# Kernel tuning notes

Measured on AMD Instinct MI355X. Metric: run time of the kernel, lower is better.

## Reference

```python
import jax, jax.numpy as jnp
import numpy as np

# Parallel-beam CT geometry constants (unit pitch, centered detector/volume)
VOXEL_W = 1.0   # voxel width (mm) == integration step along the ray
PIXEL_W = 1.0   # detector column pitch (mm)
N_T = 384       # ray samples, ~ sqrt(2) * 256 to cover the volume diagonal


def setup_inputs() -> dict:
    key = jax.random.key(0)
    vol = jax.random.normal(key, (1, 32, 256, 256), dtype=jnp.float32)  # [B, Z, Y, X]
    phis = jnp.arange(180, dtype=jnp.float32)  # view angles in degrees
    return {"vol": vol, "phis": phis}


def _project(vol, phis_deg):
    """Ray-driven parallel-beam forward projection with bilinear interpolation.

    vol: [B, Z, Y, X] attenuation volume.
    Returns sinogram g: [B, nAngles, nRows=Z, nCols=X].
    """
    B, Z, Y, X = vol.shape
    nCols = X
    dtype = vol.dtype
    centerCol = (nCols - 1) / 2.0
    # detector-column lateral offsets and ray-parameter samples (world coords)
    u = (jnp.arange(nCols, dtype=dtype) - centerCol) * PIXEL_W          # [nCols]
    t = (jnp.arange(N_T, dtype=dtype) - (N_T - 1) / 2.0) * VOXEL_W      # [nT]
    phis = phis_deg * (jnp.pi / 180.0)
    cs = jnp.stack([jnp.cos(phis), jnp.sin(phis)], axis=-1)             # [nAngles, 2]

    def bilinear(ix, iy):
        # ix, iy: fractional voxel coords, shape [nT, nCols]
        ix0f = jnp.floor(ix); iy0f = jnp.floor(iy)
        fx = ix - ix0f; fy = iy - iy0f
        ix0 = ix0f.astype(jnp.int32); iy0 = iy0f.astype(jnp.int32)
        ix1 = ix0 + 1; iy1 = iy0 + 1

        def valid_clip(i, n):
            v = (i >= 0) & (i <= n - 1)
            return v, jnp.clip(i, 0, n - 1)

        vx0, jx0 = valid_clip(ix0, X); vx1, jx1 = valid_clip(ix1, X)
        vy0, jy0 = valid_clip(iy0, Y); vy1, jy1 = valid_clip(iy1, Y)
        zero = jnp.zeros((), dtype)
        wx0 = jnp.where(vx0, 1.0 - fx, zero); wx1 = jnp.where(vx1, fx, zero)
        wy0 = jnp.where(vy0, 1.0 - fy, zero); wy1 = jnp.where(vy1, fy, zero)
        # gathers broadcast over [B, Z]; result [B, Z, nT, nCols]
        return (wy0 * (wx0 * vol[..., jy0, jx0] + wx1 * vol[..., jy0, jx1])
              + wy1 * (wx0 * vol[..., jy1, jx0] + wx1 * vol[..., jy1, jx1]))

    def one_angle(carry, cs_a):
        c, s = cs_a[0], cs_a[1]
        # world (x, y) sample positions along each detector column's ray
        x = u[None, :] * (-s) + t[:, None] * c   # [nT, nCols]
        y = u[None, :] * c + t[:, None] * s
        ix = x / VOXEL_W + (X - 1) / 2.0
        iy = y / VOXEL_W + (Y - 1) / 2.0
        vals = bilinear(ix, iy)                  # [B, Z, nT, nCols]
        g = vals.sum(axis=2) * VOXEL_W           # line integral -> [B, Z, nCols]
        return carry, g

    _, g = jax.lax.scan(one_angle, 0, cs)        # [nAngles, B, Z, nCols]
    return jnp.transpose(g, (1, 0, 2, 3))        # [B, nAngles, Z, nCols]


def reference(vol, phis):
    return _project(vol, phis)
```

## Files before the change

kernel.cpp:

```cpp
#include <hip/hip_runtime.h>
#include <hip/hip_fp16.h>

#define XDIM 256
#define YDIM 256
#define ZDIM 32
#define NT 384
#define NA 180
#define AG 2
#define SW 263
#define SR 70
#define CELLS (SR * SW)
#define SMEM_BYTES 147280

__global__ __launch_bounds__(1024) void proj_kernel(
    const float* __restrict__ vol, const float* __restrict__ phis,
    float* __restrict__ out) {
  extern __shared__ char smem[];
  uint2* sl = reinterpret_cast<uint2*>(smem);
  float4* ps = reinterpret_cast<float4*>(smem);

  const int tid = threadIdx.x;
  const int zq = blockIdx.x;
  const int ag = blockIdx.y;
  const int col = tid & 255;
  const int q = tid >> 8;
  const float u = (float)col - 127.5f;

  const float phi0 = phis[ag * AG] * 0.017453292519943295f;
  const int ax = (fabsf(sinf(phi0)) >= fabsf(cosf(phi0))) ? 1 : 0;

  float c_[AG], s_[AG];
#pragma unroll
  for (int j = 0; j < AG; ++j) {
    const float phi = phis[ag * AG + j] * 0.017453292519943295f;
    c_[j] = cosf(phi);
    s_[j] = sinf(phi);
  }
  float4 acc[AG];
#pragma unroll
  for (int j = 0; j < AG; ++j) acc[j] = make_float4(0.f, 0.f, 0.f, 0.f);

  const float* vb = vol + (zq * 4) * (YDIM * XDIM);

#pragma unroll
  for (int st = 0; st < 4; ++st) {
    const int gr0 = st * 64 - 3;
    __syncthreads();

    if (tid < SR * 7) {
      int r = tid / 7;
      int c7 = tid - r * 7;
      int lw = c7 < 3 ? c7 : c7 + 256;
      sl[r * SW + lw] = make_uint2(0u, 0u);
    }
    if (ax) {
      for (int i = 0; i < 18; ++i) {
        int k = tid + (i << 10);
        if (k < SR * 256) {
          int r = k >> 8, x = k & 255, gr = gr0 + r;
          uint2 v = make_uint2(0u, 0u);
          if ((unsigned)gr < 256u) {
            int gi = gr * XDIM + x;
            __half2 p = __floats2half2_rn(vb[gi], vb[gi + 65536]);
            __half2 qq = __floats2half2_rn(vb[gi + 131072], vb[gi + 196608]);
            v.x = *reinterpret_cast<unsigned*>(&p);
            v.y = *reinterpret_cast<unsigned*>(&qq);
          }
          sl[r * SW + x + 3] = v;
        }
      }
    } else {
      for (int i = 0; i < 16; ++i) {
        int k = tid + (i << 10);
        int r = k & 63, y = k >> 6, gx = gr0 + r;
        uint2 v = make_uint2(0u, 0u);
        if ((unsigned)gx < 256u) {
          int gi = y * XDIM + gx;
          __half2 p = __floats2half2_rn(vb[gi], vb[gi + 65536]);
          __half2 qq = __floats2half2_rn(vb[gi + 131072], vb[gi + 196608]);
          v.x = *reinterpret_cast<unsigned*>(&p);
          v.y = *reinterpret_cast<unsigned*>(&qq);
        }
        sl[r * SW + y + 3] = v;
      }
      for (int i = 0; i < 2; ++i) {
        int k = tid + (i << 10);
        int rb = k & 7, y = k >> 3;
        if (rb < 6) {
          int r = 64 + rb, gx = gr0 + r;
          uint2 v = make_uint2(0u, 0u);
          if ((unsigned)gx < 256u) {
            int gi = y * XDIM + gx;
            __half2 p = __floats2half2_rn(vb[gi], vb[gi + 65536]);
            __half2 qq = __floats2half2_rn(vb[gi + 131072], vb[gi + 196608]);
            v.x = *reinterpret_cast<unsigned*>(&p);
            v.y = *reinterpret_cast<unsigned*>(&qq);
          }
          sl[r * SW + y + 3] = v;
        }
      }
    }
    __syncthreads();

    const int KOFF = (3 - 64 * st) * SW + 3;
#pragma unroll
    for (int j = 0; j < AG; ++j) {
      const float c = c_[j], s = s_[j];
      const float bx = fmaf(u, -s, 127.5f);
      const float by = fmaf(u, c, 127.5f);
      const float cr = ax ? s : c, br = ax ? by : bx;
      const float cc = ax ? c : s, bc = ax ? bx : by;

      float t1 = (-1.f - br) / cr + 191.5f;
      float t2 = (256.f - br) / cr + 191.5f;
      float flo = fmaxf(0.f, fminf(t1, t2) - 2.f);
      float fhi = fminf((float)NT, fmaxf(t1, t2) + 2.f);
      if (fabsf(cc) < 1e-6f) {
        if (bc <= -1.f || bc >= 256.f) { flo = 1.f; fhi = 0.f; }
      } else {
        float t3 = (-1.f - bc) / cc + 191.5f;
        float t4 = (256.f - bc) / cc + 191.5f;
        flo = fmaxf(flo, fminf(t3, t4) - 2.f);
        fhi = fminf(fhi, fmaxf(t3, t4) + 2.f);
      }
      const int glo = (int)ceilf(flo);
      const int ghi = (int)fhi;

      float ta = ((float)(64 * st) - br) / cr + 191.5f;
      float tb = ((float)(64 * st + 64) - br) / cr + 191.5f;
      int ia = (int)ceilf(ta);
      int ib = (int)ceilf(tb);
      int lo, hi;
      if (cr > 0.f) {
        lo = (st == 0) ? glo : max(glo, ia);
        hi = (st == 3) ? ghi : min(ghi, ib);
      } else {
        lo = (st == 3) ? glo : max(glo, ib);
        hi = (st == 0) ? ghi : min(ghi, ia);
      }
      const int start = lo + ((q - lo) & 3);
      const int d = hi - start;
      const int n = d > 0 ? (d + 3) >> 2 : 0;
      float t = (float)start - 191.5f;
      float a0 = acc[j].x, a1 = acc[j].y, a2 = acc[j].z, a3 = acc[j].w;
#pragma unroll 2
      for (int k = 0; k < n; ++k, t += 4.f) {
        float rr = fmaf(t, cr, br);
        float ww = fmaf(t, cc, bc);
        float r0f = floorf(rr), w0f = floorf(ww);
        float fr = rr - r0f, fw = ww - w0f;
        int ai = (int)fmaf(r0f, (float)SW, w0f) + KOFF;
        uint2 D00 = sl[ai], D01 = sl[ai + 1];
        uint2 D10 = sl[ai + SW], D11 = sl[ai + SW + 1];
        __half2 fw2 = __float2half2_rn(fw);
        __half2 e00 = *reinterpret_cast<__half2*>(&D00.x);
        __half2 o00 = *reinterpret_cast<__half2*>(&D00.y);
        __half2 e01 = *reinterpret_cast<__half2*>(&D01.x);
        __half2 o01 = *reinterpret_cast<__half2*>(&D01.y);
        __half2 e10 = *reinterpret_cast<__half2*>(&D10.x);
        __half2 o10 = *reinterpret_cast<__half2*>(&D10.y);
        __half2 e11 = *reinterpret_cast<__half2*>(&D11.x);
        __half2 o11 = *reinterpret_cast<__half2*>(&D11.y);
        __half2 hxa = __hfma2(__hsub2(e01, e00), fw2, e00);
        __half2 hxb = __hfma2(__hsub2(o01, o00), fw2, o00);
        __half2 hya = __hfma2(__hsub2(e11, e10), fw2, e10);
        __half2 hyb = __hfma2(__hsub2(o11, o10), fw2, o10);
        float omfr = 1.f - fr;
        a0 = fmaf(__low2float(hxa), omfr, a0);
        a0 = fmaf(__low2float(hya), fr, a0);
        a1 = fmaf(__high2float(hxa), omfr, a1);
        a1 = fmaf(__high2float(hya), fr, a1);
        a2 = fmaf(__low2float(hxb), omfr, a2);
        a2 = fmaf(__low2float(hyb), fr, a2);
        a3 = fmaf(__high2float(hxb), omfr, a3);
        a3 = fmaf(__high2float(hyb), fr, a3);
      }
      acc[j] = make_float4(a0, a1, a2, a3);
    }
  }

#pragma unroll
  for (int j = 0; j < AG; ++j) {
    __syncthreads();
    ps[tid] = acc[j];
    __syncthreads();
    if (tid < 256) {
      float4 A = ps[col], B = ps[256 + col], C = ps[512 + col],
             D = ps[768 + col];
      const int a = ag * AG + j;
      const int zb = zq * 4;
      out[(a * ZDIM + zb + 0) * XDIM + col] = A.x + B.x + C.x + D.x;
      out[(a * ZDIM + zb + 1) * XDIM + col] = A.y + B.y + C.y + D.y;
      out[(a * ZDIM + zb + 2) * XDIM + col] = A.z + B.z + C.z + D.z;
      out[(a * ZDIM + zb + 3) * XDIM + col] = A.w + B.w + C.w + D.w;
    }
  }
}

extern "C" void kernel_launch(void* const* d_in, const int* in_sizes, int n_in,
                              void* d_out, int out_size, void* d_ws, size_t ws_size,
                              hipStream_t stream) {
  const float* vol = (const float*)d_in[0];
  const float* phis = (const float*)d_in[1];
  float* out = (float*)d_out;
  (void)hipFuncSetAttribute((const void*)proj_kernel,
                            hipFuncAttributeMaxDynamicSharedMemorySize,
                            SMEM_BYTES);
  dim3 grid(ZDIM / 4, NA / AG);
  proj_kernel<<<grid, 1024, SMEM_BYTES, stream>>>(vol, phis, out);
}
```

Before: 237.9 us.

## Double-buffer smaller LDS strips and overlap global loads with compute

```diff
diff --git a/kernel.cpp b/kernel.cpp
--- a/kernel.cpp
+++ b/kernel.cpp
@@ -8,11 +8,12 @@
 #define NA 180
 #define AG 2
 #define SW 263
-#define SR 70
-#define CELLS (SR * SW)
-#define SMEM_BYTES 147280
-
-__global__ __launch_bounds__(1024) void proj_kernel(
+#define SR 38
+#define NST 8
+#define SLICE (SR * SW)
+#define SMEM_BYTES (2 * SLICE * 8)
+
+__global__ __launch_bounds__(1024, 4) void proj_kernel(
     const float* __restrict__ vol, const float* __restrict__ phis,
     float* __restrict__ out) {
   extern __shared__ char smem[];
@@ -29,160 +30,185 @@
   const float phi0 = phis[ag * AG] * 0.017453292519943295f;
   const int ax = (fabsf(sinf(phi0)) >= fabsf(cosf(phi0))) ? 1 : 0;
 
-  float c_[AG], s_[AG];
-#pragma unroll
-  for (int j = 0; j < AG; ++j) {
-    const float phi = phis[ag * AG + j] * 0.017453292519943295f;
-    c_[j] = cosf(phi);
-    s_[j] = sinf(phi);
-  }
-  float4 acc[AG];
-#pragma unroll
-  for (int j = 0; j < AG; ++j) acc[j] = make_float4(0.f, 0.f, 0.f, 0.f);
+  const float phiB = phis[ag * AG + 1] * 0.017453292519943295f;
+  const float c0 = cosf(phi0), s0 = sinf(phi0);
+  const float c1 = cosf(phiB), s1 = sinf(phiB);
+
+  float4 acc0 = make_float4(0.f, 0.f, 0.f, 0.f);
+  float4 acc1 = make_float4(0.f, 0.f, 0.f, 0.f);
 
   const float* vb = vol + (zq * 4) * (YDIM * XDIM);
 
-#pragma unroll
-  for (int st = 0; st < 4; ++st) {
-    const int gr0 = st * 64 - 3;
-    __syncthreads();
-
-    if (tid < SR * 7) {
-      int r = tid / 7;
-      int c7 = tid - r * 7;
-      int lw = c7 < 3 ? c7 : c7 + 256;
-      sl[r * SW + lw] = make_uint2(0u, 0u);
-    }
-    if (ax) {
-      for (int i = 0; i < 18; ++i) {
-        int k = tid + (i << 10);
+  float4 fS[5];
+
+  auto LOAD = [&](int st1, int b) {
+    const int gr0 = st1 * 32 - 3;
+#pragma unroll
+    for (int i = 0; i < 5; ++i) {
+      const int ii = b * 5 + i;
+      const int k = tid + (ii << 10);
+      float4 val = make_float4(0.f, 0.f, 0.f, 0.f);
+      if (ax) {
         if (k < SR * 256) {
           int r = k >> 8, x = k & 255, gr = gr0 + r;
-          uint2 v = make_uint2(0u, 0u);
           if ((unsigned)gr < 256u) {
             int gi = gr * XDIM + x;
-            __half2 p = __floats2half2_rn(vb[gi], vb[gi + 65536]);
-            __half2 qq = __floats2half2_rn(vb[gi + 131072], vb[gi + 196608]);
-            v.x = *reinterpret_cast<unsigned*>(&p);
-            v.y = *reinterpret_cast<unsigned*>(&qq);
+            val.x = vb[gi];          val.y = vb[gi + 65536];
+            val.z = vb[gi + 131072]; val.w = vb[gi + 196608];
           }
-          sl[r * SW + x + 3] = v;
-        }
-      }
-    } else {
-      for (int i = 0; i < 16; ++i) {
-        int k = tid + (i << 10);
-        int r = k & 63, y = k >> 6, gx = gr0 + r;
-        uint2 v = make_uint2(0u, 0u);
-        if ((unsigned)gx < 256u) {
-          int gi = y * XDIM + gx;
-          __half2 p = __floats2half2_rn(vb[gi], vb[gi + 65536]);
-          __half2 qq = __floats2half2_rn(vb[gi + 131072], vb[gi + 196608]);
-          v.x = *reinterpret_cast<unsigned*>(&p);
-          v.y = *reinterpret_cast<unsigned*>(&qq);
-        }
-        sl[r * SW + y + 3] = v;
-      }
-      for (int i = 0; i < 2; ++i) {
-        int k = tid + (i << 10);
-        int rb = k & 7, y = k >> 3;
-        if (rb < 6) {
-          int r = 64 + rb, gx = gr0 + r;
-          uint2 v = make_uint2(0u, 0u);
+        }
+      } else {
+        if (ii < 8) {
+          int r = k & 31, y = k >> 5, gx = gr0 + r;
           if ((unsigned)gx < 256u) {
             int gi = y * XDIM + gx;
-            __half2 p = __floats2half2_rn(vb[gi], vb[gi + 65536]);
-            __half2 qq = __floats2half2_rn(vb[gi + 131072], vb[gi + 196608]);
-            v.x = *reinterpret_cast<unsigned*>(&p);
-            v.y = *reinterpret_cast<unsigned*>(&qq);
+            val.x = vb[gi];          val.y = vb[gi + 65536];
+            val.z = vb[gi + 131072]; val.w = vb[gi + 196608];
           }
-          sl[r * SW + y + 3] = v;
+        } else {
+          int kb = tid + ((ii - 8) << 10);
+          int rb = kb & 7, y = kb >> 3;
+          if (rb < 6) {
+            int gx = gr0 + 32 + rb;
+            if ((unsigned)gx < 256u) {
+              int gi = y * XDIM + gx;
+              val.x = vb[gi];          val.y = vb[gi + 65536];
+              val.z = vb[gi + 131072]; val.w = vb[gi + 196608];
+            }
+          }
         }
       }
-    }
+      fS[i] = val;
+    }
+  };
+
+  auto WRITE = [&](int st1, int b) {
+    uint2* buf = sl + (st1 & 1) * SLICE;
+#pragma unroll
+    for (int i = 0; i < 5; ++i) {
+      const int ii = b * 5 + i;
+      const int k = tid + (ii << 10);
+      __half2 p = __floats2half2_rn(fS[i].x, fS[i].y);
+      __half2 qq = __floats2half2_rn(fS[i].z, fS[i].w);
+      uint2 val;
+      val.x = *reinterpret_cast<unsigned*>(&p);
+      val.y = *reinterpret_cast<unsigned*>(&qq);
+      if (ax) {
+        if (k < SR * 256) {
+          int r = k >> 8, x = k & 255;
+          buf[r * SW + x + 3] = val;
+        }
+      } else {
+        if (ii < 8) {
+          int r = k & 31, y = k >> 5;
+          buf[r * SW + y + 3] = val;
+        } else {
+          int kb = tid + ((ii - 8) << 10);
+          int rb = kb & 7, y = kb >> 3;
+          if (rb < 6) buf[(32 + rb) * SW + y + 3] = val;
+        }
+      }
+    }
+  };
+
+  auto COMPUTE = [&](int st, float c, float s, float4& A) {
+    const int KOFF = (3 - 32 * st) * SW + 3 + (st & 1) * SLICE;
+    const float bx = fmaf(u, -s, 127.5f);
+    const float by = fmaf(u, c, 127.5f);
+    const float cr = ax ? s : c, br = ax ? by : bx;
+    const float cc = ax ? c : s, bc = ax ? bx : by;
+    float t1 = (-1.f - br) / cr + 191.5f;
+    float t2 = (256.f - br) / cr + 191.5f;
+    float flo = fmaxf(0.f, fminf(t1, t2) - 2.f);
+    float fhi = fminf((float)NT, fmaxf(t1, t2) + 2.f);
+    if (fabsf(cc) < 1e-6f) {
+      if (bc <= -1.f || bc >= 256.f) { flo = 1.f; fhi = 0.f; }
+    } else {
+      float t3 = (-1.f - bc) / cc + 191.5f;
+      float t4 = (256.f - bc) / cc + 191.5f;
+      flo = fmaxf(flo, fminf(t3, t4) - 2.f);
+      fhi = fminf(fhi, fmaxf(t3, t4) + 2.f);
+    }
+    const int glo = (int)ceilf(flo);
+    const int ghi = (int)fhi;
+    float ta = ((float)(32 * st) - br) / cr + 191.5f;
+    float tb = ((float)(32 * st + 32) - br) / cr + 191.5f;
+    int ia = (int)ceilf(ta);
+    int ib = (int)ceilf(tb);
+    int lo, hi;
+    if (cr > 0.f) {
+      lo = (st == 0) ? glo : max(glo, ia);
+      hi = (st == NST - 1) ? ghi : min(ghi, ib);
+    } else {
+      lo = (st == NST - 1) ? glo : max(glo, ib);
+      hi = (st == 0) ? ghi : min(ghi, ia);
+    }
+    const int start = lo + ((q - lo) & 3);
+    const int d = hi - start;
+    const int n = d > 0 ? (d + 3) >> 2 : 0;
+    float t = (float)start - 191.5f;
+    float a0 = A.x, a1 = A.y, a2 = A.z, a3 = A.w;
+#pragma unroll 2
+    for (int k2 = 0; k2 < n; ++k2, t += 4.f) {
+      float rr = fmaf(t, cr, br);
+      float ww = fmaf(t, cc, bc);
+      float r0f = floorf(rr), w0f = floorf(ww);
+      float fr = rr - r0f, fw = ww - w0f;
+      int ai = (int)fmaf(r0f, (float)SW, w0f) + KOFF;
+      uint2 D00 = sl[ai], D01 = sl[ai + 1];
+      uint2 D10 = sl[ai + SW], D11 = sl[ai + SW + 1];
+      __half2 fw2 = __float2half2_rn(fw);
+      __half2 e00 = *reinterpret_cast<__half2*>(&D00.x);
+      __half2 o00 = *reinterpret_cast<__half2*>(&D00.y);
+      __half2 e01 = *reinterpret_cast<__half2*>(&D01.x);
+      __half2 o01 = *reinterpret_cast<__half2*>(&D01.y);
+      __half2 e10 = *reinterpret_cast<__half2*>(&D10.x);
+      __half2 o10 = *reinterpret_cast<__half2*>(&D10.y);
+      __half2 e11 = *reinterpret_cast<__half2*>(&D11.x);
+      __half2 o11 = *reinterpret_cast<__half2*>(&D11.y);
+      __half2 hxa = __hfma2(__hsub2(e01, e00), fw2, e00);
+      __half2 hxb = __hfma2(__hsub2(o01, o00), fw2, o00);
+      __half2 hya = __hfma2(__hsub2(e11, e10), fw2, e10);
+      __half2 hyb = __hfma2(__hsub2(o11, o10), fw2, o10);
+      float omfr = 1.f - fr;
+      a0 = fmaf(__low2float(hxa), omfr, a0);
+      a0 = fmaf(__low2float(hya), fr, a0);
+      a1 = fmaf(__high2float(hxa), omfr, a1);
+      a1 = fmaf(__high2float(hya), fr, a1);
+      a2 = fmaf(__low2float(hxb), omfr, a2);
+      a2 = fmaf(__low2float(hyb), fr, a2);
+      a3 = fmaf(__high2float(hxb), omfr, a3);
+      a3 = fmaf(__high2float(hyb), fr, a3);
+    }
+    A = make_float4(a0, a1, a2, a3);
+  };
+
+  if (tid < 2 * SR * 7) {
+    int bi = tid / (SR * 7);
+    int rr2 = tid - bi * (SR * 7);
+    int r = rr2 / 7;
+    int c7 = rr2 - r * 7;
+    int lw = c7 < 3 ? c7 : c7 + 256;
+    sl[bi * SLICE + r * SW + lw] = make_uint2(0u, 0u);
+  }
+  LOAD(0, 0); WRITE(0, 0);
+  LOAD(0, 1); WRITE(0, 1);
+  __syncthreads();
+
+#pragma unroll
+  for (int st = 0; st < NST; ++st) {
+    if (st < NST - 1) LOAD(st + 1, 0);
+    COMPUTE(st, c0, s0, acc0);
+    if (st < NST - 1) { WRITE(st + 1, 0); LOAD(st + 1, 1); }
+    COMPUTE(st, c1, s1, acc1);
+    if (st < NST - 1) WRITE(st + 1, 1);
     __syncthreads();
-
-    const int KOFF = (3 - 64 * st) * SW + 3;
-#pragma unroll
-    for (int j = 0; j < AG; ++j) {
-      const float c = c_[j], s = s_[j];
-      const float bx = fmaf(u, -s, 127.5f);
-      const float by = fmaf(u, c, 127.5f);
-      const float cr = ax ? s : c, br = ax ? by : bx;
-      const float cc = ax ? c : s, bc = ax ? bx : by;
-
-      float t1 = (-1.f - br) / cr + 191.5f;
-      float t2 = (256.f - br) / cr + 191.5f;
-      float flo = fmaxf(0.f, fminf(t1, t2) - 2.f);
-      float fhi = fminf((float)NT, fmaxf(t1, t2) + 2.f);
-      if (fabsf(cc) < 1e-6f) {
-        if (bc <= -1.f || bc >= 256.f) { flo = 1.f; fhi = 0.f; }
-      } else {
-        float t3 = (-1.f - bc) / cc + 191.5f;
-        float t4 = (256.f - bc) / cc + 191.5f;
-        flo = fmaxf(flo, fminf(t3, t4) - 2.f);
-        fhi = fminf(fhi, fmaxf(t3, t4) + 2.f);
-      }
-      const int glo = (int)ceilf(flo);
-      const int ghi = (int)fhi;
-
-      float ta = ((float)(64 * st) - br) / cr + 191.5f;
-      float tb = ((float)(64 * st + 64) - br) / cr + 191.5f;
-      int ia = (int)ceilf(ta);
-      int ib = (int)ceilf(tb);
-      int lo, hi;
-      if (cr > 0.f) {
-        lo = (st == 0) ? glo : max(glo, ia);
-        hi = (st == 3) ? ghi : min(ghi, ib);
-      } else {
-        lo = (st == 3) ? glo : max(glo, ib);
-        hi = (st == 0) ? ghi : min(ghi, ia);
-      }
-      const int start = lo + ((q - lo) & 3);
-      const int d = hi - start;
-      const int n = d > 0 ? (d + 3) >> 2 : 0;
-      float t = (float)start - 191.5f;
-      float a0 = acc[j].x, a1 = acc[j].y, a2 = acc[j].z, a3 = acc[j].w;
-#pragma unroll 2
-      for (int k = 0; k < n; ++k, t += 4.f) {
-        float rr = fmaf(t, cr, br);
-        float ww = fmaf(t, cc, bc);
-        float r0f = floorf(rr), w0f = floorf(ww);
-        float fr = rr - r0f, fw = ww - w0f;
-        int ai = (int)fmaf(r0f, (float)SW, w0f) + KOFF;
-        uint2 D00 = sl[ai], D01 = sl[ai + 1];
-        uint2 D10 = sl[ai + SW], D11 = sl[ai + SW + 1];
-        __half2 fw2 = __float2half2_rn(fw);
-        __half2 e00 = *reinterpret_cast<__half2*>(&D00.x);
-        __half2 o00 = *reinterpret_cast<__half2*>(&D00.y);
-        __half2 e01 = *reinterpret_cast<__half2*>(&D01.x);
-        __half2 o01 = *reinterpret_cast<__half2*>(&D01.y);
-        __half2 e10 = *reinterpret_cast<__half2*>(&D10.x);
-        __half2 o10 = *reinterpret_cast<__half2*>(&D10.y);
-        __half2 e11 = *reinterpret_cast<__half2*>(&D11.x);
-        __half2 o11 = *reinterpret_cast<__half2*>(&D11.y);
-        __half2 hxa = __hfma2(__hsub2(e01, e00), fw2, e00);
-        __half2 hxb = __hfma2(__hsub2(o01, o00), fw2, o00);
-        __half2 hya = __hfma2(__hsub2(e11, e10), fw2, e10);
-        __half2 hyb = __hfma2(__hsub2(o11, o10), fw2, o10);
-        float omfr = 1.f - fr;
-        a0 = fmaf(__low2float(hxa), omfr, a0);
-        a0 = fmaf(__low2float(hya), fr, a0);
-        a1 = fmaf(__high2float(hxa), omfr, a1);
-        a1 = fmaf(__high2float(hya), fr, a1);
-        a2 = fmaf(__low2float(hxb), omfr, a2);
-        a2 = fmaf(__low2float(hyb), fr, a2);
-        a3 = fmaf(__high2float(hxb), omfr, a3);
-        a3 = fmaf(__high2float(hyb), fr, a3);
-      }
-      acc[j] = make_float4(a0, a1, a2, a3);
-    }
   }
 
 #pragma unroll
   for (int j = 0; j < AG; ++j) {
     __syncthreads();
-    ps[tid] = acc[j];
+    ps[tid] = j ? acc1 : acc0;
     __syncthreads();
     if (tid < 256) {
       float4 A = ps[col], B = ps[256 + col], C = ps[512 + col],
```

Result: slower. 244.6 us (+2.8%).
